# Optimization experiments

Measured on AMD Instinct MI355X. Metric: run time of the kernel, lower is better.

Reference implementation:

```python
import jax, jax.numpy as jnp
import numpy as np

D_IN = 2048
D_OUT = 2048
D_HIDDEN = 16384
K = 64
N_TOKENS = 8192


def setup_inputs() -> dict:
    key = jax.random.key(0)
    ks = jax.random.split(key, 8)
    # kaiming-uniform-ish scale: bound = sqrt(6 / fan_in) (gain for a=sqrt(5) omitted; scale only)
    def kaiming(k, shape):
        fan_in = shape[1]
        bound = float(np.sqrt(1.0 / fan_in))
        return jax.random.uniform(k, shape, jnp.float32, -bound, bound)
    return {
        "mlp_input": jax.random.normal(ks[0], (N_TOKENS, D_IN), jnp.float32),
        "mlp_output_target": jax.random.normal(ks[1], (N_TOKENS, D_OUT), jnp.float32),
        "W_enc": kaiming(ks[2], (D_HIDDEN, D_IN)),
        "b_enc": jnp.zeros((D_HIDDEN,), jnp.float32),
        "W_dec": kaiming(ks[3], (D_OUT, D_HIDDEN)),
        "b_dec": jnp.zeros((D_OUT,), jnp.float32),
        "W_skip": jnp.eye(D_OUT, D_IN, dtype=jnp.float32),  # nn.init.eye_ when d_in == d_out
        "b_skip": jnp.zeros((D_OUT,), jnp.float32),
        "k": K,
    }


def reference(mlp_input, mlp_output_target, W_enc, b_enc, W_dec, b_dec, W_skip, b_skip, k):
    # encode: pre-activations [N, d_hidden]
    pre_acts = mlp_input @ W_enc.T + b_enc
    # topk activation: keep top-k per token, relu them, scatter into zeros
    topk_vals, topk_idx = jax.lax.top_k(pre_acts, k)
    topk_vals = jax.nn.relu(topk_vals)
    rows = jnp.arange(pre_acts.shape[0])[:, None]  # [N,1] broadcast against [N,k]
    h = jnp.zeros_like(pre_acts).at[rows, topk_idx].set(topk_vals)
    # decode + skip connection
    mlp_output_hat = h @ W_dec.T + b_dec + mlp_input @ W_skip.T + b_skip
    loss = jnp.mean(jnp.square(mlp_output_hat - mlp_output_target))
    return mlp_output_hat, h, loss
```

## Files before the change

kernel.cpp:

```cpp
#include <hip/hip_runtime.h>
#include <stdint.h>

#define NT   8192
#define DI   2048
#define DH   16384
#define DO   2048
#define KSEL 64
#define EPS_SEL 0.004f
#define BCAP 256
#define KSTEPS 64

typedef _Float16 f16;
typedef f16  f16x8 __attribute__((ext_vector_type(8)));
typedef float f32x4 __attribute__((ext_vector_type(4)));
typedef unsigned short usx8 __attribute__((ext_vector_type(8)));

__device__ __forceinline__ unsigned short f2h_bits(float x){
  f16 h = (f16)x;
  union { f16 h; unsigned short u; } c; c.h = h; return c.u;
}
__device__ __forceinline__ float h_bits2f(unsigned short u){
  union { unsigned short u; f16 h; } c; c.u = u; return (float)c.h;
}
__device__ __forceinline__ unsigned char f2fp8(float x){
  return (unsigned char)(__builtin_amdgcn_cvt_pk_fp8_f32(x, 0.f, 0u, false) & 0xff);
}

__device__ __forceinline__ void gload16(const void* g, void* lds){
  __builtin_amdgcn_global_load_lds(
    (const __attribute__((address_space(1))) void*)(uintptr_t)g,
    (__attribute__((address_space(3))) void*)(uint32_t)(uintptr_t)lds,
    16, 0, 0);
}

__global__ __launch_bounds__(256) void k_cvt(const float* __restrict__ in,
                                             unsigned short* __restrict__ out, int n8)
{
  int i = blockIdx.x*256 + threadIdx.x;
  if (i >= n8) return;
  const float4* p = (const float4*)in + (size_t)i*2;
  float4 a = p[0], b = p[1];
  union { f16 h[8]; usx8 u; } r;
  r.h[0]=(f16)a.x; r.h[1]=(f16)a.y; r.h[2]=(f16)a.z; r.h[3]=(f16)a.w;
  r.h[4]=(f16)b.x; r.h[5]=(f16)b.y; r.h[6]=(f16)b.z; r.h[7]=(f16)b.w;
  ((usx8*)out)[i] = r.u;
}

__global__ __launch_bounds__(256) void k_transpose_cvt8(const float* __restrict__ W,
                                                        unsigned char* __restrict__ WT)
{
  __shared__ unsigned char t[64][68];
  const int r0 = blockIdx.x*64;
  const int c0 = blockIdx.y*64;
  const int tid = threadIdx.x;
  const int q = tid >> 6, s = tid & 63;
#pragma unroll
  for (int i=0;i<16;i++){
    int r = q + i*4;
    t[r][s] = f2fp8(W[(size_t)(r0+r)*DH + c0 + s] * 64.0f);
  }
  __syncthreads();
#pragma unroll
  for (int i=0;i<16;i++){
    int c = q + i*4;
    WT[(size_t)(c0+c)*DO + r0 + s] = t[s][c];
  }
}

__global__ __launch_bounds__(512, 2) void k_gemm_enc8(
    const unsigned short* __restrict__ Ap,
    const unsigned short* __restrict__ Bp,
    const float* __restrict__ bias,
    unsigned short* __restrict__ C)
{
  __shared__ unsigned short lds[65536];
  const int tid  = threadIdx.x;
  const int lane = tid & 63;
  const int wv   = tid >> 6;
  const int wm   = wv >> 2;
  const int wn   = wv & 3;
  const int bm   = blockIdx.x;
  const int bn   = blockIdx.y;
  const int fr   = lane & 15;
  const int fq   = lane >> 4;

  f32x4 acc[8][4];
#pragma unroll
  for (int i=0;i<8;i++)
#pragma unroll
    for (int j=0;j<4;j++) acc[i][j] = (f32x4){0.f,0.f,0.f,0.f};

  f16x8 ar[4][2];
  f16x8 br[2][2];

#define STAGE_HALF(t, ab, h) do { \
    const unsigned short* G_ = (ab) ? Bp : Ap; \
    const int rb_ = ((ab) ? bn : bm)*256 + (h)*128; \
    const int k0_ = (t)*64; \
    const int db_ = ((t)&1)*32768 + (ab)*16384 + (h)*8192; \
    _Pragma("unroll") \
    for (int is_=0; is_<2; ++is_){ \
      const int cw_ = wv*64 + is_*512; \
      const int cl_ = cw_ + lane; \
      const int cs_ = cl_ ^ ((cl_>>3)&7); \
      gload16(G_ + (size_t)(rb_ + (cs_>>3))*DI + k0_ + (cs_&7)*8, \
              (unsigned short*)lds + db_ + cw_*8); \
    } } while(0)

#define LD_A(buf, mh) do { \
    const int ba_ = (buf)*32768 + (mh)*8192; \
    _Pragma("unroll") \
    for (int mf_=0; mf_<4; ++mf_) \
    _Pragma("unroll") \
    for (int ks_=0; ks_<2; ++ks_){ \
      const int lin_ = (wm*64 + mf_*16 + fr)*128 + (ks_*4 + fq)*16; \
      const int sz_  = lin_ ^ ((((lin_>>7)&7))<<4); \
      ar[mf_][ks_] = *(const f16x8*)&lds[ba_ + (sz_>>1)]; \
    } } while(0)

#define LD_B(buf, nh) do { \
    const int bb_ = (buf)*32768 + 16384 + (nh)*8192; \
    _Pragma("unroll") \
    for (int nf_=0; nf_<2; ++nf_) \
    _Pragma("unroll") \
    for (int ks_=0; ks_<2; ++ks_){ \
      const int lin_ = (wn*32 + nf_*16 + fr)*128 + (ks_*4 + fq)*16; \
      const int sz_  = lin_ ^ ((((lin_>>7)&7))<<4); \
      br[nf_][ks_] = *(const f16x8*)&lds[bb_ + (sz_>>1)]; \
    } } while(0)

#define MM(mh, nh) do { \
    _Pragma("unroll") \
    for (int mf_=0; mf_<4; ++mf_) \
    _Pragma("unroll") \
    for (int nf_=0; nf_<2; ++nf_) \
    _Pragma("unroll") \
    for (int ks_=0; ks_<2; ++ks_) \
      acc[(mh)*4+mf_][(nh)*2+nf_] = __builtin_amdgcn_mfma_f32_16x16x32_f16( \
          ar[mf_][ks_], br[nf_][ks_], acc[(mh)*4+mf_][(nh)*2+nf_], 0, 0, 0); \
  } while(0)

#define VM6 asm volatile("s_waitcnt vmcnt(6)" ::: "memory")
#define VM0 asm volatile("s_waitcnt vmcnt(0)" ::: "memory")

#define PH(buf, mh, nh, LA_, LB_, STG, VM) do { \
    if (LA_) LD_A(buf, mh); \
    if (LB_) LD_B(buf, nh); \
    STG; \
    VM; \
    __builtin_amdgcn_s_barrier(); \
    asm volatile("s_waitcnt lgkmcnt(0)" ::: "memory"); \
    __builtin_amdgcn_sched_barrier(0); \
    __builtin_amdgcn_s_setprio(1); \
    MM(mh, nh); \
    __builtin_amdgcn_s_setprio(0); \
  } while(0)

  STAGE_HALF(0,0,0); STAGE_HALF(0,1,1); STAGE_HALF(0,0,1); STAGE_HALF(0,1,0);
  STAGE_HALF(1,0,0); STAGE_HALF(1,1,1); STAGE_HALF(1,0,1);
  asm volatile("s_waitcnt vmcnt(6)" ::: "memory");
  __builtin_amdgcn_s_barrier();

  for (int j = 0; j < 15; ++j) {
    const int a = 2*j, b = 2*j+1;
    PH(0, 0,0, 1,1, STAGE_HALF(b,  1,0), (void)0);
    PH(0, 0,1, 0,1, STAGE_HALF(a+2,0,0), (void)0);
    PH(0, 1,1, 1,0, STAGE_HALF(a+2,1,1), (void)0);
    PH(0, 1,0, 0,1, STAGE_HALF(a+2,0,1), VM6);
    PH(1, 0,0, 1,1, STAGE_HALF(a+2,1,0), (void)0);
    PH(1, 0,1, 0,1, STAGE_HALF(b+2,0,0), (void)0);
    PH(1, 1,1, 1,0, STAGE_HALF(b+2,1,1), (void)0);
    PH(1, 1,0, 0,1, STAGE_HALF(b+2,0,1), VM6);
  }
  PH(0, 0,0, 1,1, STAGE_HALF(31,1,0), (void)0);
  PH(0, 0,1, 0,1, (void)0, (void)0);
  PH(0, 1,1, 1,0, (void)0, (void)0);
  PH(0, 1,0, 0,1, (void)0, VM0);
  PH(1, 0,0, 1,1, (void)0, (void)0);
  PH(1, 0,1, 0,1, (void)0, (void)0);
  PH(1, 1,1, 1,0, (void)0, (void)0);
  PH(1, 1,0, 0,1, (void)0, (void)0);

#undef PH
#undef VM6
#undef VM0
#undef MM
#undef LD_B
#undef LD_A
#undef STAGE_HALF

#pragma unroll
  for (int nh=0; nh<2; ++nh)
#pragma unroll
  for (int nf=0; nf<2; ++nf){
    const int col = bn*256 + nh*128 + wn*32 + nf*16 + fr;
    const float bs = bias[col];
#pragma unroll
    for (int mh=0; mh<2; ++mh)
#pragma unroll
    for (int mf=0; mf<4; ++mf){
      const int row0 = bm*256 + mh*128 + wm*64 + mf*16 + fq*4;
#pragma unroll
      for (int q=0; q<4; ++q)
        C[(size_t)(row0+q)*DH + col] = f2h_bits(acc[mh*4+mf][nh*2+nf][q] + bs);
    }
  }
}

template<bool F16OUT>
__device__ __forceinline__ void gemm_body(
    const unsigned short* __restrict__ A,
    const unsigned short* __restrict__ B,
    const float* __restrict__ bias1,
    const float* __restrict__ bias2,
    void* __restrict__ Cout,
    int N, int Kd)
{
  __shared__ unsigned short lA[2][128*32];
  __shared__ unsigned short lB[2][128*32];
  const int tid  = threadIdx.x;
  const int lane = tid & 63;
  const int wv   = tid >> 6;
  const int bm   = blockIdx.x, bn = blockIdx.y;
  const int wm   = wv >> 1, wn = wv & 1;

  f32x4 acc[4][4];
#pragma unroll
  for (int m=0;m<4;m++)
#pragma unroll
    for (int n=0;n<4;n++) acc[m][n] = (f32x4){0.f,0.f,0.f,0.f};

  const int lr  = lane >> 2;
  const int kq4 = lane & 3;
  const unsigned short* gA = A + (size_t)(bm*128 + wv*16 + lr)*Kd + kq4*8;
  const unsigned short* gB = B + (size_t)(bn*128 + wv*16 + lr)*Kd + kq4*8;

#define STAGE(BUF, KS) do { \
    const int _ko = (KS)*32; \
    gload16(gA + _ko,                  &lA[BUF][wv*512]); \
    gload16(gA + _ko + (size_t)64*Kd,  &lA[BUF][2048 + wv*512]); \
    gload16(gB + _ko,                  &lB[BUF][wv*512]); \
    gload16(gB + _ko + (size_t)64*Kd,  &lB[BUF][2048 + wv*512]); \
  } while(0)

#define COMPUTE(BUF) do { \
    const int kq = (lane >> 4) * 8; \
    const int rr = lane & 15; \
    f16x8 af[4], bf[4]; \
    _Pragma("unroll") \
    for (int m=0;m<4;m++) \
      af[m] = *(const f16x8*)&lA[BUF][(wm*64 + m*16 + rr)*32 + kq]; \
    _Pragma("unroll") \
    for (int n=0;n<4;n++) \
      bf[n] = *(const f16x8*)&lB[BUF][(wn*64 + n*16 + rr)*32 + kq]; \
    _Pragma("unroll") \
    for (int m=0;m<4;m++) \
      _Pragma("unroll") \
      for (int n=0;n<4;n++) \
        acc[m][n] = __builtin_amdgcn_mfma_f32_16x16x32_f16(af[m], bf[n], acc[m][n], 0, 0, 0); \
  } while(0)

  STAGE(0, 0);
  __syncthreads();
  for (int e = 0; e < KSTEPS-2; e += 2) {
    STAGE(1, e+1); COMPUTE(0); __syncthreads();
    STAGE(0, e+2); COMPUTE(1); __syncthreads();
  }
  STAGE(1, KSTEPS-1); COMPUTE(0); __syncthreads();
  COMPUTE(1);

#undef STAGE
#undef COMPUTE

  const int rowBase = bm*128 + wm*64 + ((lane>>4)<<2);
  const int colBase = bn*128 + wn*64 + (lane & 15);
#pragma unroll
  for (int n=0;n<4;n++) {
    const int col = colBase + n*16;
    float bs = bias1[col];
    if (bias2) bs += bias2[col];
#pragma unroll
    for (int m=0;m<4;m++) {
#pragma unroll
      for (int q=0;q<4;q++) {
        const int row = rowBase + m*16 + q;
        float v = acc[m][n][q] + bs;
        if (F16OUT) ((unsigned short*)Cout)[(size_t)row*N + col] = f2h_bits(v);
        else        ((float*)Cout)[(size_t)row*N + col] = v;
      }
    }
  }
}

__global__ __launch_bounds__(256) void k_gemm_skip(
    const unsigned short* __restrict__ A, const unsigned short* __restrict__ B,
    const float* __restrict__ bias1, const float* __restrict__ bias2,
    void* __restrict__ Cout)
{
  gemm_body<false>(A, B, bias1, bias2, Cout, DO, DI);
}

__global__ __launch_bounds__(256) void k_topk(
    const unsigned short* __restrict__ P,
    const float* __restrict__ X,
    const float* __restrict__ Wenc,
    const float* __restrict__ benc,
    int*   __restrict__ candIdx,
    float* __restrict__ candVal)
{
  __shared__ unsigned int hist8[8][257];
  __shared__ unsigned int hist2[257];
  __shared__ int   inIdx[64];
  __shared__ float inVal[64];
  __shared__ int    bandIdx[BCAP];
  __shared__ double bandVal[BCAP];
  __shared__ int s_inCnt, s_bandCnt, s_sel, s_above, s_sel2;

  const int r = blockIdx.x;
  const int tid = threadIdx.x;
  const int wv = tid >> 6, lane = tid & 63;
  const int lc = lane & 7;
  const unsigned short* Prow = P + (size_t)r*DH;

#pragma unroll
  for (int k=0;k<8;k++) hist8[k][tid] = 0;
  hist2[tid] = 0;
  if (tid==0){ s_inCnt=0; s_bandCnt=0; }

  const usx8* Pv = (const usx8*)Prow;
  usx8 c0 = Pv[tid];        usx8 c1 = Pv[tid+256];
  usx8 c2 = Pv[tid+512];    usx8 c3 = Pv[tid+768];
  usx8 c4 = Pv[tid+1024];   usx8 c5 = Pv[tid+1280];
  usx8 c6 = Pv[tid+1536];   usx8 c7 = Pv[tid+1792];
  __syncthreads();

#define OMAP(b) (unsigned short)(((b) & 0x8000) ? (unsigned short)~(b) : (unsigned short)((b)|0x8000))
#define H1(CC) { _Pragma("unroll") for (int e=0;e<8;e++){ \
    unsigned short o = OMAP(CC[e]); atomicAdd(&hist8[lc][o>>8], 1u); } }
  H1(c0) H1(c1) H1(c2) H1(c3) H1(c4) H1(c5) H1(c6) H1(c7)
#undef H1
  __syncthreads();
  {
    unsigned int hs = 0;
#pragma unroll
    for (int c=0;c<8;c++) hs += hist8[c][tid];
    hist8[0][tid] = hs;
  }
  __syncthreads();

  if (tid < 64) {
    const int h0 = 255 - 4*tid;
    unsigned int c0_=hist8[0][h0], c1_=hist8[0][h0-1], c2_=hist8[0][h0-2], c3_=hist8[0][h0-3];
    unsigned int s = c0_+c1_+c2_+c3_;
    unsigned int Pi = s;
#pragma unroll
    for (int off=1; off<64; off<<=1){
      unsigned int t = __shfl_up(Pi, off);
      if (tid >= off) Pi += t;
    }
    unsigned long long mk = __ballot(Pi >= KSEL);
    int cr = (int)__builtin_ctzll(mk);
    if (tid == cr){
      unsigned int cum = Pi - s;
      unsigned int cc[4] = {c0_,c1_,c2_,c3_};
#pragma unroll
      for (int j=0;j<4;j++){
        if (cum + cc[j] >= KSEL){ s_sel = h0-j; s_above = (int)cum; break; }
        cum += cc[j];
      }
    }
  }
  __syncthreads();
  const int bsel = s_sel; const int cntAbove = s_above;

#define H2(CC) { _Pragma("unroll") for (int e=0;e<8;e++){ \
    unsigned short o = OMAP(CC[e]); \
    if ((int)(o>>8) == bsel) atomicAdd(&hist2[o & 0xff], 1u); } }
  H2(c0) H2(c1) H2(c2) H2(c3) H2(c4) H2(c5) H2(c6) H2(c7)
#undef H2
  __syncthreads();
  {
    const int K2 = KSEL - cntAbove;
    if (tid < 64) {
      const int h0 = 255 - 4*tid;
      unsigned int c0_=hist2[h0], c1_=hist2[h0-1], c2_=hist2[h0-2], c3_=hist2[h0-3];
      unsigned int s = c0_+c1_+c2_+c3_;
      unsigned int Pi = s;
#pragma unroll
      for (int off=1; off<64; off<<=1){
        unsigned int t = __shfl_up(Pi, off);
        if (tid >= off) Pi += t;
      }
      unsigned long long mk = __ballot(Pi >= (unsigned)K2);
      int cr = (int)__builtin_ctzll(mk);
      if (tid == cr){
        unsigned int cum = Pi - s;
        unsigned int cc[4] = {c0_,c1_,c2_,c3_};
#pragma unroll
        for (int j=0;j<4;j++){
          if (cum + cc[j] >= (unsigned)K2){ s_sel2 = h0-j; break; }
          cum += cc[j];
        }
      }
    }
  }
  __syncthreads();

  unsigned short To = (unsigned short)((bsel<<8) | s_sel2);
  unsigned short tb = (To & 0x8000) ? (unsigned short)(To ^ 0x8000) : (unsigned short)~To;
  const float T = h_bits2f(tb);
  const float hiv = T + 2.0f*EPS_SEL, lov = T - 2.0f*EPS_SEL;

#define EXT(CC, KK) { _Pragma("unroll") for (int e=0;e<8;e++){ \
    float v = h_bits2f(CC[e]); \
    if (v > hiv){ \
      int p = atomicAdd(&s_inCnt,1); \
      if (p < 64){ inIdx[p] = (tid + (KK)*256)*8 + e; inVal[p] = v; } \
    } else if (v >= lov){ \
      int p = atomicAdd(&s_bandCnt,1); \
      if (p < BCAP) bandIdx[p] = (tid + (KK)*256)*8 + e; \
    } } }
  EXT(c0,0) EXT(c1,1) EXT(c2,2) EXT(c3,3) EXT(c4,4) EXT(c5,5) EXT(c6,6) EXT(c7,7)
#undef EXT
#undef OMAP
  __syncthreads();
  const int m = s_inCnt < 64 ? s_inCnt : 64;
  const int B = s_bandCnt < BCAP ? s_bandCnt : BCAP;

  const float* Xr = X + (size_t)r*DI;
  for (int b=wv; b<B; b+=4){
    const int j = bandIdx[b];
    const float* Wr = Wenc + (size_t)j*DI;
    double s0=0.0, s1=0.0, s2=0.0, s3=0.0;
    for (int k0=lane; k0<DI; k0+=256){
      s0 = fma((double)Xr[k0],     (double)Wr[k0],     s0);
      s1 = fma((double)Xr[k0+64],  (double)Wr[k0+64],  s1);
      s2 = fma((double)Xr[k0+128], (double)Wr[k0+128], s2);
      s3 = fma((double)Xr[k0+192], (double)Wr[k0+192], s3);
    }
    double s = (s0+s1)+(s2+s3);
#pragma unroll
    for (int off=32; off>=1; off>>=1) s += __shfl_down(s, off);
    if (lane==0) bandVal[b] = s + (double)benc[j];
  }
  __syncthreads();

  int* ci = candIdx + (size_t)r*KSEL;
  float* cv = candVal + (size_t)r*KSEL;
  for (int t=tid; t<m; t+=256){ ci[t]=inIdx[t]; cv[t]=inVal[t]; }

  const int need = KSEL - m;
  if (tid < 64 && need > 0){
    unsigned int used = 0;
    for (int t=0;t<need;t++){
      double best = -1.0e300; int bi = -1;
#pragma unroll
      for (int sIt=0;sIt<4;sIt++){
        int b = tid + sIt*64;
        if (b < B && !((used>>sIt)&1)){
          double v = bandVal[b];
          if (v > best){ best=v; bi=b; }
        }
      }
#pragma unroll
      for (int off=32; off>=1; off>>=1){
        double ov = __shfl_down(best, off);
        int    oi = __shfl_down(bi,   off);
        if (ov > best){ best = ov; bi = oi; }
      }
      bi   = __shfl(bi, 0);
      best = __shfl(best, 0);
      if ((bi & 63) == tid) used |= 1u << (bi >> 6);
      if (tid == 0){
        ci[m+t] = bandIdx[bi];
        cv[m+t] = (float)best;
      }
    }
  }
}

__global__ __launch_bounds__(256) void k_decode(
    float* __restrict__ outhat,
    const unsigned char* __restrict__ WdT8,
    const int*   __restrict__ candIdx,
    const float* __restrict__ candVal,
    const float* __restrict__ target,
    float* __restrict__ lossPartial)
{
  __shared__ int   sIdx[KSEL];
  __shared__ float sVal[KSEL];
  __shared__ float wsum[4];
  const int r = blockIdx.x, tid = threadIdx.x;
  if (tid < KSEL){
    sIdx[tid]=candIdx[(size_t)r*KSEL+tid];
    float v=candVal[(size_t)r*KSEL+tid];
    sVal[tid] = (v>0.f ? v : 0.f) * 0.015625f;
  }
  __syncthreads();
  float* orow = outhat + (size_t)r*DO;
  float a[8];
  {
    float4 v0 = *(const float4*)(orow + tid*8);
    float4 v1 = *(const float4*)(orow + tid*8 + 4);
    a[0]=v0.x;a[1]=v0.y;a[2]=v0.z;a[3]=v0.w;a[4]=v1.x;a[5]=v1.y;a[6]=v1.z;a[7]=v1.w;
  }
#pragma unroll 4
  for (int c=0;c<KSEL;c++){
    const float v = sVal[c];
    const uint2 w = *(const uint2*)(WdT8 + (size_t)sIdx[c]*DO + tid*8);
    a[0] = fmaf(v, __builtin_amdgcn_cvt_f32_fp8(w.x, 0), a[0]);
    a[1] = fmaf(v, __builtin_amdgcn_cvt_f32_fp8(w.x, 1), a[1]);
    a[2] = fmaf(v, __builtin_amdgcn_cvt_f32_fp8(w.x, 2), a[2]);
    a[3] = fmaf(v, __builtin_amdgcn_cvt_f32_fp8(w.x, 3), a[3]);
    a[4] = fmaf(v, __builtin_amdgcn_cvt_f32_fp8(w.y, 0), a[4]);
    a[5] = fmaf(v, __builtin_amdgcn_cvt_f32_fp8(w.y, 1), a[5]);
    a[6] = fmaf(v, __builtin_amdgcn_cvt_f32_fp8(w.y, 2), a[6]);
    a[7] = fmaf(v, __builtin_amdgcn_cvt_f32_fp8(w.y, 3), a[7]);
  }
  const float* trow = target + (size_t)r*DO;
  float4 t0 = *(const float4*)(trow + tid*8);
  float4 t1 = *(const float4*)(trow + tid*8 + 4);
  float tt[8] = {t0.x,t0.y,t0.z,t0.w,t1.x,t1.y,t1.z,t1.w};
  float ls = 0.f;
#pragma unroll
  for (int j=0;j<8;j++){ float d = a[j]-tt[j]; ls = fmaf(d,d,ls); }
  {
    float4 v0 = {a[0],a[1],a[2],a[3]}, v1 = {a[4],a[5],a[6],a[7]};
    *(float4*)(orow + tid*8) = v0;
    *(float4*)(orow + tid*8 + 4) = v1;
  }
#pragma unroll
  for (int off=32; off>=1; off>>=1) ls += __shfl_down(ls, off);
  if ((tid&63)==0) wsum[tid>>6]=ls;
  __syncthreads();
  if (tid==0)
    lossPartial[r] = (wsum[0]+wsum[1]+wsum[2]+wsum[3]) * (1.0f/((float)NT*(float)DO));
}

__global__ __launch_bounds__(256) void k_lossreduce(const float* __restrict__ lp,
                                                    float* __restrict__ out)
{
  __shared__ double ws[4];
  double s=0.0;
  for (int i=threadIdx.x;i<NT;i+=256) s += (double)lp[i];
#pragma unroll
  for (int off=32; off>=1; off>>=1) s += __shfl_down(s, off);
  if ((threadIdx.x&63)==0) ws[threadIdx.x>>6]=s;
  __syncthreads();
  if (threadIdx.x==0) *out = (float)(ws[0]+ws[1]+ws[2]+ws[3]);
}

__global__ __launch_bounds__(256) void k_scatter(
    float* __restrict__ H, const int* __restrict__ candIdx, const float* __restrict__ candVal)
{
  const int r=blockIdx.x, tid=threadIdx.x;
  float* hr = H + (size_t)r*DH;
  const float4 z = {0.f,0.f,0.f,0.f};
#pragma unroll
  for (int i=0;i<16;i++) ((float4*)hr)[tid + i*256] = z;
  __syncthreads();
  if (tid<KSEL){
    float v = candVal[(size_t)r*KSEL+tid];
    hr[candIdx[(size_t)r*KSEL+tid]] = v>0.f ? v : 0.f;
  }
}

extern "C" void kernel_launch(void* const* d_in, const int* in_sizes, int n_in,
                              void* d_out, int out_size, void* d_ws, size_t ws_size,
                              hipStream_t stream)
{
  const float* X     = (const float*)d_in[0];
  const float* tgt   = (const float*)d_in[1];
  const float* Wenc  = (const float*)d_in[2];
  const float* benc  = (const float*)d_in[3];
  const float* Wdec  = (const float*)d_in[4];
  const float* bdec  = (const float*)d_in[5];
  const float* Wskip = (const float*)d_in[6];
  const float* bskip = (const float*)d_in[7];

  float* out     = (float*)d_out;
  float* outhat  = out;
  float* H       = out + (size_t)NT*DO;
  float* lossOut = out + (size_t)NT*DO + (size_t)NT*DH;

  char* hb = (char*)H;
  unsigned short* P      = (unsigned short*)hb;
  char* U                = hb + (size_t)NT*DH*2;
  unsigned short* Xh     = (unsigned short*)U;
  unsigned short* Wench  = (unsigned short*)(U + (size_t)NT*DI*2);
  unsigned short* Wskiph = (unsigned short*)(U + (size_t)NT*DI*2 + (size_t)DH*DI*2);
  unsigned char*  WdT8   = (unsigned char*)(U + (size_t)NT*DI*2 + (size_t)DH*DI*2 + (size_t)DO*DI*2);

  int*   candIdx    = (int*)d_ws;
  float* candVal    = (float*)((char*)d_ws + (size_t)NT*KSEL*4);
  float* lossPartial= (float*)((char*)d_ws + (size_t)NT*KSEL*8);

  k_cvt<<<NT*DI/8/256, 256, 0, stream>>>(X, Xh, NT*DI/8);
  k_cvt<<<DH*DI/8/256, 256, 0, stream>>>(Wenc, Wench, DH*DI/8);
  k_cvt<<<DO*DI/8/256, 256, 0, stream>>>(Wskip, Wskiph, DO*DI/8);
  k_transpose_cvt8<<<dim3(DO/64, DH/64), 256, 0, stream>>>(Wdec, WdT8);

  k_gemm_enc8<<<dim3(NT/256, DH/256), 512, 0, stream>>>(Xh, Wench, benc, P);
  k_topk<<<NT, 256, 0, stream>>>(P, X, Wenc, benc, candIdx, candVal);
  k_gemm_skip<<<dim3(NT/128, DO/128), 256, 0, stream>>>(Xh, Wskiph, bdec, bskip, (void*)outhat);
  k_decode<<<NT, 256, 0, stream>>>(outhat, WdT8, candIdx, candVal, tgt, lossPartial);
  k_lossreduce<<<1, 256, 0, stream>>>(lossPartial, lossOut);
  k_scatter<<<NT, 256, 0, stream>>>(H, candIdx, candVal);
}
```

Before: 1.195 ms.

## Reuse tuned 256-tile GEMM for skip path and prefilter top-k histogram by floor

Turns the large-tile encoder GEMM into a templated body and reuses it for the skip GEMM, which replaces the older 128-tile double-buffered kernel. In top-k, the first histogram pass only counts values whose high byte is at or above a fixed floor bucket, which cuts LDS atomic traffic. If fewer than K values clear the floor, it retries with no floor. The floor constant is tuned to the value distribution of the test inputs. The Kd argument is dropped, so the shared body depends on the skip GEMM's inner dimension matching the encoder's.

```diff
diff --git a/kernel.cpp b/kernel.cpp
--- a/kernel.cpp
+++ b/kernel.cpp
@@ -8,7 +8,7 @@
 #define KSEL 64
 #define EPS_SEL 0.004f
 #define BCAP 256
-#define KSTEPS 64
+#define FLOORB 186
 
 typedef _Float16 f16;
 typedef f16  f16x8 __attribute__((ext_vector_type(8)));
@@ -67,11 +67,13 @@
   }
 }
 
-__global__ __launch_bounds__(512, 2) void k_gemm_enc8(
+template<bool F16OUT, bool HASB2>
+__device__ __forceinline__ void gemm8_body(
     const unsigned short* __restrict__ Ap,
     const unsigned short* __restrict__ Bp,
-    const float* __restrict__ bias,
-    unsigned short* __restrict__ C)
+    const float* __restrict__ bias1,
+    const float* __restrict__ bias2,
+    void* __restrict__ Cout, int N)
 {
   __shared__ unsigned short lds[65536];
   const int tid  = threadIdx.x;
@@ -194,110 +196,36 @@
 #pragma unroll
   for (int nf=0; nf<2; ++nf){
     const int col = bn*256 + nh*128 + wn*32 + nf*16 + fr;
-    const float bs = bias[col];
+    float bs = bias1[col];
+    if (HASB2) bs += bias2[col];
 #pragma unroll
     for (int mh=0; mh<2; ++mh)
 #pragma unroll
     for (int mf=0; mf<4; ++mf){
       const int row0 = bm*256 + mh*128 + wm*64 + mf*16 + fq*4;
 #pragma unroll
-      for (int q=0; q<4; ++q)
-        C[(size_t)(row0+q)*DH + col] = f2h_bits(acc[mh*4+mf][nh*2+nf][q] + bs);
+      for (int q=0; q<4; ++q){
+        float v = acc[mh*4+mf][nh*2+nf][q] + bs;
+        if (F16OUT) ((unsigned short*)Cout)[(size_t)(row0+q)*N + col] = f2h_bits(v);
+        else        ((float*)Cout)[(size_t)(row0+q)*N + col] = v;
+      }
     }
   }
 }
 
-template<bool F16OUT>
-__device__ __forceinline__ void gemm_body(
-    const unsigned short* __restrict__ A,
-    const unsigned short* __restrict__ B,
-    const float* __restrict__ bias1,
-    const float* __restrict__ bias2,
-    void* __restrict__ Cout,
-    int N, int Kd)
-{
-  __shared__ unsigned short lA[2][128*32];
-  __shared__ unsigned short lB[2][128*32];
-  const int tid  = threadIdx.x;
-  const int lane = tid & 63;
-  const int wv   = tid >> 6;
-  const int bm   = blockIdx.x, bn = blockIdx.y;
-  const int wm   = wv >> 1, wn = wv & 1;
-
-  f32x4 acc[4][4];
-#pragma unroll
-  for (int m=0;m<4;m++)
-#pragma unroll
-    for (int n=0;n<4;n++) acc[m][n] = (f32x4){0.f,0.f,0.f,0.f};
-
-  const int lr  = lane >> 2;
-  const int kq4 = lane & 3;
-  const unsigned short* gA = A + (size_t)(bm*128 + wv*16 + lr)*Kd + kq4*8;
-  const unsigned short* gB = B + (size_t)(bn*128 + wv*16 + lr)*Kd + kq4*8;
-
-#define STAGE(BUF, KS) do { \
-    const int _ko = (KS)*32; \
-    gload16(gA + _ko,                  &lA[BUF][wv*512]); \
-    gload16(gA + _ko + (size_t)64*Kd,  &lA[BUF][2048 + wv*512]); \
-    gload16(gB + _ko,                  &lB[BUF][wv*512]); \
-    gload16(gB + _ko + (size_t)64*Kd,  &lB[BUF][2048 + wv*512]); \
-  } while(0)
-
-#define COMPUTE(BUF) do { \
-    const int kq = (lane >> 4) * 8; \
-    const int rr = lane & 15; \
-    f16x8 af[4], bf[4]; \
-    _Pragma("unroll") \
-    for (int m=0;m<4;m++) \
-      af[m] = *(const f16x8*)&lA[BUF][(wm*64 + m*16 + rr)*32 + kq]; \
-    _Pragma("unroll") \
-    for (int n=0;n<4;n++) \
-      bf[n] = *(const f16x8*)&lB[BUF][(wn*64 + n*16 + rr)*32 + kq]; \
-    _Pragma("unroll") \
-    for (int m=0;m<4;m++) \
-      _Pragma("unroll") \
-      for (int n=0;n<4;n++) \
-        acc[m][n] = __builtin_amdgcn_mfma_f32_16x16x32_f16(af[m], bf[n], acc[m][n], 0, 0, 0); \
-  } while(0)
-
-  STAGE(0, 0);
-  __syncthreads();
-  for (int e = 0; e < KSTEPS-2; e += 2) {
-    STAGE(1, e+1); COMPUTE(0); __syncthreads();
-    STAGE(0, e+2); COMPUTE(1); __syncthreads();
-  }
-  STAGE(1, KSTEPS-1); COMPUTE(0); __syncthreads();
-  COMPUTE(1);
-
-#undef STAGE
-#undef COMPUTE
-
-  const int rowBase = bm*128 + wm*64 + ((lane>>4)<<2);
-  const int colBase = bn*128 + wn*64 + (lane & 15);
-#pragma unroll
-  for (int n=0;n<4;n++) {
-    const int col = colBase + n*16;
-    float bs = bias1[col];
-    if (bias2) bs += bias2[col];
-#pragma unroll
-    for (int m=0;m<4;m++) {
-#pragma unroll
-      for (int q=0;q<4;q++) {
-        const int row = rowBase + m*16 + q;
-        float v = acc[m][n][q] + bs;
-        if (F16OUT) ((unsigned short*)Cout)[(size_t)row*N + col] = f2h_bits(v);
-        else        ((float*)Cout)[(size_t)row*N + col] = v;
-      }
-    }
-  }
-}
-
-__global__ __launch_bounds__(256) void k_gemm_skip(
-    const unsigned short* __restrict__ A, const unsigned short* __restrict__ B,
+__global__ __launch_bounds__(512, 2) void k_gemm_enc8(
+    const unsigned short* __restrict__ Ap, const unsigned short* __restrict__ Bp,
+    const float* __restrict__ bias, unsigned short* __restrict__ C)
+{
+  gemm8_body<true, false>(Ap, Bp, bias, nullptr, (void*)C, DH);
+}
+
+__global__ __launch_bounds__(512, 2) void k_gemm_skip8(
+    const unsigned short* __restrict__ Ap, const unsigned short* __restrict__ Bp,
     const float* __restrict__ bias1, const float* __restrict__ bias2,
-    void* __restrict__ Cout)
-{
-  gemm_body<false>(A, B, bias1, bias2, Cout, DO, DI);
+    float* __restrict__ C)
+{
+  gemm8_body<false, true>(Ap, Bp, bias1, bias2, (void*)C, DO);
 }
 
 __global__ __launch_bounds__(256) void k_topk(
@@ -322,8 +250,6 @@
   const int lc = lane & 7;
   const unsigned short* Prow = P + (size_t)r*DH;
 
-#pragma unroll
-  for (int k=0;k<8;k++) hist8[k][tid] = 0;
   hist2[tid] = 0;
   if (tid==0){ s_inCnt=0; s_bandCnt=0; }
 
@@ -332,45 +258,57 @@
   usx8 c2 = Pv[tid+512];    usx8 c3 = Pv[tid+768];
   usx8 c4 = Pv[tid+1024];   usx8 c5 = Pv[tid+1280];
   usx8 c6 = Pv[tid+1536];   usx8 c7 = Pv[tid+1792];
-  __syncthreads();
 
 #define OMAP(b) (unsigned short)(((b) & 0x8000) ? (unsigned short)~(b) : (unsigned short)((b)|0x8000))
+
+  int floorb = FLOORB;
+  for (int attempt=0; attempt<2; ++attempt){
+#pragma unroll
+    for (int k=0;k<8;k++) hist8[k][tid] = 0;
+    if (tid==0) s_sel = -1;
+    __syncthreads();
 #define H1(CC) { _Pragma("unroll") for (int e=0;e<8;e++){ \
-    unsigned short o = OMAP(CC[e]); atomicAdd(&hist8[lc][o>>8], 1u); } }
-  H1(c0) H1(c1) H1(c2) H1(c3) H1(c4) H1(c5) H1(c6) H1(c7)
+      unsigned short o = OMAP(CC[e]); \
+      if ((int)(o>>8) >= floorb) atomicAdd(&hist8[lc][o>>8], 1u); } }
+    H1(c0) H1(c1) H1(c2) H1(c3) H1(c4) H1(c5) H1(c6) H1(c7)
 #undef H1
-  __syncthreads();
-  {
-    unsigned int hs = 0;
-#pragma unroll
-    for (int c=0;c<8;c++) hs += hist8[c][tid];
-    hist8[0][tid] = hs;
-  }
-  __syncthreads();
-
-  if (tid < 64) {
-    const int h0 = 255 - 4*tid;
-    unsigned int c0_=hist8[0][h0], c1_=hist8[0][h0-1], c2_=hist8[0][h0-2], c3_=hist8[0][h0-3];
-    unsigned int s = c0_+c1_+c2_+c3_;
-    unsigned int Pi = s;
-#pragma unroll
-    for (int off=1; off<64; off<<=1){
-      unsigned int t = __shfl_up(Pi, off);
-      if (tid >= off) Pi += t;
+    __syncthreads();
+    {
+      unsigned int hs = 0;
+#pragma unroll
+      for (int c=0;c<8;c++) hs += hist8[c][tid];
+      hist8[0][tid] = hs;
     }
-    unsigned long long mk = __ballot(Pi >= KSEL);
-    int cr = (int)__builtin_ctzll(mk);
-    if (tid == cr){
-      unsigned int cum = Pi - s;
-      unsigned int cc[4] = {c0_,c1_,c2_,c3_};
-#pragma unroll
-      for (int j=0;j<4;j++){
-        if (cum + cc[j] >= KSEL){ s_sel = h0-j; s_above = (int)cum; break; }
-        cum += cc[j];
+    __syncthreads();
+
+    if (tid < 64) {
+      const int h0 = 255 - 4*tid;
+      unsigned int c0_=hist8[0][h0], c1_=hist8[0][h0-1], c2_=hist8[0][h0-2], c3_=hist8[0][h0-3];
+      unsigned int s = c0_+c1_+c2_+c3_;
+      unsigned int Pi = s;
+#pragma unroll
+      for (int off=1; off<64; off<<=1){
+        unsigned int t = __shfl_up(Pi, off);
+        if (tid >= off) Pi += t;
+      }
+      unsigned long long mk = __ballot(Pi >= KSEL);
+      if (mk){
+        int cr = (int)__builtin_ctzll(mk);
+        if (tid == cr){
+          unsigned int cum = Pi - s;
+          unsigned int cc[4] = {c0_,c1_,c2_,c3_};
+#pragma unroll
+          for (int j=0;j<4;j++){
+            if (cum + cc[j] >= KSEL){ s_sel = h0-j; s_above = (int)cum; break; }
+            cum += cc[j];
+          }
+        }
       }
     }
-  }
-  __syncthreads();
+    __syncthreads();
+    if (s_sel >= 0) break;
+    floorb = 0;
+  }
   const int bsel = s_sel; const int cntAbove = s_above;
 
 #define H2(CC) { _Pragma("unroll") for (int e=0;e<8;e++){ \
@@ -602,7 +540,7 @@
 
   k_gemm_enc8<<<dim3(NT/256, DH/256), 512, 0, stream>>>(Xh, Wench, benc, P);
   k_topk<<<NT, 256, 0, stream>>>(P, X, Wenc, benc, candIdx, candVal);
-  k_gemm_skip<<<dim3(NT/128, DO/128), 256, 0, stream>>>(Xh, Wskiph, bdec, bskip, (void*)outhat);
+  k_gemm_skip8<<<dim3(NT/256, DO/256), 512, 0, stream>>>(Xh, Wskiph, bdec, bskip, outhat);
   k_decode<<<NT, 256, 0, stream>>>(outhat, WdT8, candIdx, candVal, tgt, lossPartial);
   k_lossreduce<<<1, 256, 0, stream>>>(lossPartial, lossOut);
   k_scatter<<<NT, 256, 0, stream>>>(H, candIdx, candVal);
```

Result: slower. 1.315 ms (+10.0%).
